# Kernel tuning notes

Measured on AMD Instinct MI355X. Metric: run time of the kernel, lower is better.

Reference implementation:

```python
import jax, jax.numpy as jnp
import numpy as np

N, F_IN, F_OUT, H = 4096, 128, 64, 8
NEG_SLOPE = 0.2

def leaky_relu(x):
    return jnp.where(x >= 0, x, NEG_SLOPE * x)

def setup_inputs() -> dict:
    key = jax.random.key(0)
    k = jax.random.split(key, 6)
    x = jax.random.normal(k[0], (N, F_IN), dtype=jnp.float32)
    conn = jax.random.uniform(k[1], (N, N)) < 0.1
    conn = conn | jnp.eye(N, dtype=bool)
    topology = jnp.where(conn, 0.0, -1e9).astype(jnp.float32)
    proj = jax.random.normal(k[2], (H, F_IN, F_OUT), dtype=jnp.float32) * (1.0 / np.sqrt(F_IN))
    score_src = jax.random.normal(k[3], (H, F_OUT), dtype=jnp.float32) * (1.0 / np.sqrt(F_OUT))
    score_dst = jax.random.normal(k[4], (H, F_OUT), dtype=jnp.float32) * (1.0 / np.sqrt(F_OUT))
    skip_w = jax.random.normal(k[5], (H * F_OUT, F_IN), dtype=jnp.float32) * (1.0 / np.sqrt(F_IN))
    return {"x": x, "topology": topology, "proj": proj,
            "score_src": score_src, "score_dst": score_dst, "skip_w": skip_w}

def reference(x, topology, proj, score_src, score_dst, skip_w):
    # dropout is identity at inference time
    # projected node features: [H, N, F_OUT]
    h = jnp.einsum('ni,hio->hno', x, proj)
    # additive attention scores (GAT): [H, N, 1] + [H, 1, N] -> [H, N, N]
    s_src = jnp.einsum('hno,ho->hn', h, score_src)
    s_dst = jnp.einsum('hno,ho->hn', h, score_dst)
    scores = leaky_relu(s_src[:, :, None] + s_dst[:, None, :])
    attn = jax.nn.softmax(scores + topology[None, :, :], axis=-1)  # [H, N, N]
    # aggregate neighbors, then transpose heads to [N, H, F_OUT]
    out = jnp.einsum('hij,hjo->iho', attn, h)
    # skip connection (F_OUT != F_IN -> projected skip)
    out = out + (x @ skip_w.T).reshape(N, H, F_OUT)
    # mean over heads (concat_heads=False), then LeakyReLU activation
    out = leaky_relu(jnp.mean(out, axis=1))  # [N, F_OUT]
    return out
```

## Files before the change

kernel.cpp:

```cpp
#include <hip/hip_runtime.h>
#include <hip/hip_bf16.h>

#define NN 4096
#define FIN 128
#define FOUT 64
#define NH 8
#define KS 4
#define QT 32

typedef float f32x4 __attribute__((ext_vector_type(4)));
typedef __bf16 bf16x8 __attribute__((ext_vector_type(8)));
typedef unsigned long long u64;

__global__ __launch_bounds__(256) void wc_kernel(
    const float* __restrict__ proj, const float* __restrict__ score_src,
    const float* __restrict__ score_dst, const float* __restrict__ skip_w,
    float* __restrict__ Wc) {
    int idx = blockIdx.x * 256 + threadIdx.x;
    if (idx >= FIN * 80) return;
    int i = idx / 80, c = idx % 80;
    float v = 0.f;
    if (c < 16) {
        int h = c & 7;
        const float* w = (c < 8 ? score_src : score_dst) + h * FOUT;
        const float* p = proj + (size_t)h * FIN * FOUT + (size_t)i * FOUT;
        for (int f = 0; f < FOUT; ++f) v += p[f] * w[f];
    } else {
        int f = c - 16;
        for (int h = 0; h < NH; ++h) v += skip_w[(size_t)(h * FOUT + f) * FIN + i];
        v *= 0.125f;
    }
    Wc[i * 80 + c] = v;
}

__global__ __launch_bounds__(256) void scores_kernel(
    const float* __restrict__ x, const float* __restrict__ Wc,
    float* __restrict__ skipm, unsigned* __restrict__ EF, float2* __restrict__ C12,
    __hip_bfloat16* __restrict__ xb_) {
    __shared__ float wcs[FIN][80];
    __shared__ float xs[16][FIN + 5];
    const int n0 = blockIdx.x * 16;
    const int tid = threadIdx.x;
    for (int i = tid; i < FIN * 80 / 4; i += 256)
        ((float4*)&wcs[0][0])[i] = ((const float4*)Wc)[i];
    const float4* xsrc = (const float4*)(x + (size_t)n0 * FIN);
    for (int i = tid; i < 16 * FIN / 4; i += 256) {
        int r = i >> 5, c4 = i & 31;
        *(float4*)&xs[r][c4 * 4] = xsrc[i];
    }
    __syncthreads();
    const int r = tid & 15;
    const int g = tid >> 4;
    float acc[4];
    float sa = 0.f;
#pragma unroll
    for (int j = 0; j < 4; ++j) acc[j] = 0.f;
#pragma unroll 4
    for (int i = 0; i < FIN; ++i) {
        float xv = xs[r][i];
        float4 p = *(float4*)&wcs[i][16 + g * 4];
        float qv = wcs[i][g];
        acc[0] += xv * p.x; acc[1] += xv * p.y; acc[2] += xv * p.z; acc[3] += xv * p.w;
        sa += xv * qv;
    }
    int n = n0 + r;
#pragma unroll
    for (int j = 0; j < 4; ++j) skipm[(size_t)n * FOUT + g * 4 + j] = acc[j];
    if (g < 8) {
        C12[g * NN + n] = make_float2(expf(sa), expf(0.2f * sa));
    } else {
        __hip_bfloat16 e0 = __float2bfloat16(expf(sa));
        __hip_bfloat16 f0 = __float2bfloat16(expf(0.2f * sa));
        EF[(g - 8) * NN + n] = ((unsigned)*(unsigned short*)&f0 << 16) | (unsigned)*(unsigned short*)&e0;
    }
    {
        int row = tid >> 4, col0 = (tid & 15) * 8;
        const float* src = &xs[row][col0];
        bf16x8 b0;
#pragma unroll
        for (int j = 0; j < 8; ++j) b0[j] = (__bf16)src[j];
        *(bf16x8*)((__bf16*)xb_ + (size_t)(n0 + row) * FIN + col0) = b0;
    }
}

__global__ __launch_bounds__(256) void mask_kernel(
    const float* __restrict__ topo, u64* __restrict__ mb) {
    const int w = blockIdx.x * 4 + (threadIdx.x >> 6);
    const int lane = threadIdx.x & 63;
    size_t base = (size_t)w * 32;
#pragma unroll 4
    for (int it = 0; it < 32; ++it) {
        size_t u = base + it;
        float t = topo[u * 64 + lane];
        u64 b = __ballot(t > -0.5e9f);
        if (lane == 0) mb[u] = b;
    }
}

__global__ __launch_bounds__(256) void vt_kernel(
    const float* __restrict__ proj, const __hip_bfloat16* __restrict__ xb_,
    __hip_bfloat16* __restrict__ Vt_) {
    __shared__ __bf16 pT[FOUT][FIN + 8];
    const int tid = threadIdx.x;
    const int h = blockIdx.x >> 6;
    const int ng = blockIdx.x & 63;
    const __bf16* xb = (const __bf16*)xb_;
    __bf16* Vt = (__bf16*)Vt_;
    for (int idx = tid; idx < FIN * FOUT; idx += 256) {
        int i = idx >> 6, f = idx & 63;
        pT[f][i] = (__bf16)proj[(size_t)h * FIN * FOUT + idx];
    }
    __syncthreads();
    const int wave = tid >> 6, lane = tid & 63, q = lane >> 4, li = lane & 15;
    const int nb = ng * 64 + wave * 16;
    f32x4 acc[4];
#pragma unroll
    for (int n = 0; n < 4; ++n) acc[n] = (f32x4){0.f, 0.f, 0.f, 0.f};
#pragma unroll
    for (int kt = 0; kt < 4; ++kt) {
        bf16x8 bfrag = *(const bf16x8*)(xb + (size_t)(nb + li) * FIN + kt * 32 + q * 8);
#pragma unroll
        for (int ft = 0; ft < 4; ++ft) {
            bf16x8 afrag = *(const bf16x8*)&pT[ft * 16 + li][kt * 32 + q * 8];
            acc[ft] = __builtin_amdgcn_mfma_f32_16x16x32_bf16(afrag, bfrag, acc[ft], 0, 0, 0);
        }
    }
#pragma unroll
    for (int ft = 0; ft < 4; ++ft)
#pragma unroll
        for (int reg = 0; reg < 4; ++reg)
            Vt[((size_t)h * FOUT + ft * 16 + q * 4 + reg) * NN + nb + li] = (__bf16)acc[ft][reg];
}

__attribute__((amdgpu_waves_per_eu(4, 4)))
__global__ __launch_bounds__(512) void attn_kernel(
    const u64* __restrict__ maskbits, const __hip_bfloat16* __restrict__ Vt_,
    const unsigned* __restrict__ EFg, const float2* __restrict__ C12g,
    __hip_bfloat16* __restrict__ accP, float* __restrict__ rsP) {
    __shared__ u64 maskS[QT][17];
    const int tid = threadIdx.x;
    const int h = tid >> 6;
    const int lane = tid & 63, q = lane >> 4, li = lane & 15;
    const int qt = blockIdx.x >> 2, ks = blockIdx.x & 3;
    const int row0 = qt * QT;
    const int kb0 = ks * 1024;

    {
        int r = tid >> 4, wd = tid & 15;
        maskS[r][wd] = maskbits[(size_t)(row0 + r) * 64 + ks * 16 + wd];
    }
    __syncthreads();

    const __bf16* vb = (const __bf16*)Vt_ + (size_t)h * (FOUT * NN) + kb0;
    const unsigned* efb = EFg + (size_t)h * NN + kb0;
    float C1[2], C2[2];
#pragma unroll
    for (int rt = 0; rt < 2; ++rt) {
        float2 c = C12g[(size_t)h * NN + row0 + rt * 16 + li];
        C1[rt] = c.x; C2[rt] = c.y;
    }

    f32x4 acc[2][4];
#pragma unroll
    for (int rt = 0; rt < 2; ++rt)
#pragma unroll
        for (int n = 0; n < 4; ++n) acc[rt][n] = (f32x4){0.f, 0.f, 0.f, 0.f};
    float rs[2] = {0.f, 0.f};

#pragma unroll 1
    for (int kt = 0; kt < 32; ++kt) {
        const unsigned* ep = efb + kt * 32 + q * 8;
        uint4 ea = *(const uint4*)ep;
        uint4 eb = *(const uint4*)(ep + 4);
        bf16x8 vf[4];
#pragma unroll
        for (int n = 0; n < 4; ++n)
            vf[n] = *(const bf16x8*)(vb + (size_t)(n * 16 + li) * NN + kt * 32 + q * 8);
        unsigned ew[8] = {ea.x, ea.y, ea.z, ea.w, eb.x, eb.y, eb.z, eb.w};
#pragma unroll
        for (int rt = 0; rt < 2; ++rt) {
            u64 mw = maskS[rt * 16 + li][kt >> 1];
            unsigned mm = (unsigned)(mw >> ((kt & 1) * 32 + q * 8)) & 0xffu;
            bf16x8 pf;
#pragma unroll
            for (int j = 0; j < 8; ++j) {
                unsigned e = ew[j];
                float E = __uint_as_float(e << 16);
                float F = __uint_as_float(e & 0xffff0000u);
                float pv = fmaxf(C1[rt] * E, C2[rt] * F);
                pv = ((mm >> j) & 1u) ? pv : 0.f;
                rs[rt] += pv;
                pf[j] = (__bf16)pv;
            }
#pragma unroll
            for (int n = 0; n < 4; ++n)
                acc[rt][n] = __builtin_amdgcn_mfma_f32_16x16x32_bf16(pf, vf[n], acc[rt][n], 0, 0, 0);
        }
    }

#pragma unroll
    for (int rt = 0; rt < 2; ++rt) {
        float r = rs[rt];
        r += __shfl_xor(r, 16);
        r += __shfl_xor(r, 32);
        if (q == 0) rsP[(size_t)(ks * NH + h) * NN + row0 + rt * 16 + li] = r;
        __hip_bfloat16* ap = accP + ((size_t)(ks * NH + h) * NN + row0 + rt * 16) * 64;
#pragma unroll
        for (int n = 0; n < 4; ++n)
#pragma unroll
            for (int reg = 0; reg < 4; ++reg)
                ap[(q * 4 + reg) * 64 + n * 16 + li] = __float2bfloat16(acc[rt][n][reg]);
    }
}

__global__ __launch_bounds__(256) void combine_kernel(
    const __hip_bfloat16* __restrict__ accP, const float* __restrict__ rsP,
    float* __restrict__ out) {
    int idx = blockIdx.x * 256 + threadIdx.x;
    int row = idx >> 6, f = idx & 63;
    float s = 0.f;
#pragma unroll 1
    for (int h = 0; h < NH; ++h) {
        float a = 0.f, r = 0.f;
#pragma unroll
        for (int k = 0; k < KS; ++k) {
            a += __bfloat162float(accP[((size_t)(k * NH + h) * NN + row) * 64 + f]);
            r += rsP[(size_t)(k * NH + h) * NN + row];
        }
        s += a / r;
    }
    float v = s * 0.125f + out[idx];
    out[idx] = fmaxf(v, 0.2f * v);
}

extern "C" void kernel_launch(void* const* d_in, const int* in_sizes, int n_in,
                              void* d_out, int out_size, void* d_ws, size_t ws_size,
                              hipStream_t stream) {
    (void)in_sizes; (void)n_in; (void)out_size; (void)ws_size;
    const float* x         = (const float*)d_in[0];
    const float* topology  = (const float*)d_in[1];
    const float* proj      = (const float*)d_in[2];
    const float* score_src = (const float*)d_in[3];
    const float* score_dst = (const float*)d_in[4];
    const float* skip_w    = (const float*)d_in[5];
    float* out = (float*)d_out;

    char* ws = (char*)d_ws;
    __hip_bfloat16* xb = (__hip_bfloat16*)ws;
    __hip_bfloat16* Vt = (__hip_bfloat16*)(ws + 1048576);
    unsigned* EF  = (unsigned*)(ws + 5242880);
    float2* C12   = (float2*)(ws + 5373952);
    float* Wc     = (float*)(ws + 5636096);
    u64* maskbits = (u64*)(ws + 5677056);
    float* rsP    = (float*)(ws + 7774208);
    __hip_bfloat16* accP = (__hip_bfloat16*)(ws + 8298496);
    float* skipm = out;

    wc_kernel<<<40, 256, 0, stream>>>(proj, score_src, score_dst, skip_w, Wc);
    scores_kernel<<<256, 256, 0, stream>>>(x, Wc, skipm, EF, C12, xb);
    mask_kernel<<<2048, 256, 0, stream>>>(topology, maskbits);
    vt_kernel<<<512, 256, 0, stream>>>(proj, xb, Vt);
    attn_kernel<<<512, 512, 0, stream>>>(maskbits, Vt, EF, C12, accP, rsP);
    combine_kernel<<<1024, 256, 0, stream>>>(accP, rsP, out);
}
```

Measured before the change: 209.5 us.

## Fuse mask bit-packing into attention kernel and double-buffer K-tile loads

Removes the separate mask_kernel: each attention block now reads its 32x1024 slice of the fp32 topology directly and ballots it into shared-memory bitmasks, so the packed mask buffer no longer makes a round trip through global memory and one launch is dropped. The main K loop is also software-pipelined with two register buffers, so the EF and V loads for the next tile are issued before the current tile's compute. The risks are higher register pressure under the fixed waves-per-eu setting, and the topology read now sitting serialized at the start of every attention block (64 iterations per wave, unroll 1). Workspace offsets are compacted to match.

```diff
diff --git a/kernel.cpp b/kernel.cpp
--- a/kernel.cpp
+++ b/kernel.cpp
@@ -83,20 +83,6 @@
     }
 }
 
-__global__ __launch_bounds__(256) void mask_kernel(
-    const float* __restrict__ topo, u64* __restrict__ mb) {
-    const int w = blockIdx.x * 4 + (threadIdx.x >> 6);
-    const int lane = threadIdx.x & 63;
-    size_t base = (size_t)w * 32;
-#pragma unroll 4
-    for (int it = 0; it < 32; ++it) {
-        size_t u = base + it;
-        float t = topo[u * 64 + lane];
-        u64 b = __ballot(t > -0.5e9f);
-        if (lane == 0) mb[u] = b;
-    }
-}
-
 __global__ __launch_bounds__(256) void vt_kernel(
     const float* __restrict__ proj, const __hip_bfloat16* __restrict__ xb_,
     __hip_bfloat16* __restrict__ Vt_) {
@@ -134,7 +120,7 @@
 
 __attribute__((amdgpu_waves_per_eu(4, 4)))
 __global__ __launch_bounds__(512) void attn_kernel(
-    const u64* __restrict__ maskbits, const __hip_bfloat16* __restrict__ Vt_,
+    const float* __restrict__ topo, const __hip_bfloat16* __restrict__ Vt_,
     const unsigned* __restrict__ EFg, const float2* __restrict__ C12g,
     __hip_bfloat16* __restrict__ accP, float* __restrict__ rsP) {
     __shared__ u64 maskS[QT][17];
@@ -146,8 +132,14 @@
     const int kb0 = ks * 1024;
 
     {
-        int r = tid >> 4, wd = tid & 15;
-        maskS[r][wd] = maskbits[(size_t)(row0 + r) * 64 + ks * 16 + wd];
+        const float* tpb = topo + (size_t)row0 * NN + kb0;
+#pragma unroll 1
+        for (int it = 0; it < 64; ++it) {
+            int w0 = h * 64 + it;
+            float t = tpb[(size_t)(w0 >> 4) * NN + (w0 & 15) * 64 + lane];
+            u64 b = __ballot(t > -0.5e9f);
+            if (lane == 0) maskS[w0 >> 4][w0 & 15] = b;
+        }
     }
     __syncthreads();
 
@@ -167,16 +159,18 @@
         for (int n = 0; n < 4; ++n) acc[rt][n] = (f32x4){0.f, 0.f, 0.f, 0.f};
     float rs[2] = {0.f, 0.f};
 
-#pragma unroll 1
-    for (int kt = 0; kt < 32; ++kt) {
-        const unsigned* ep = efb + kt * 32 + q * 8;
-        uint4 ea = *(const uint4*)ep;
-        uint4 eb = *(const uint4*)(ep + 4);
-        bf16x8 vf[4];
-#pragma unroll
-        for (int n = 0; n < 4; ++n)
-            vf[n] = *(const bf16x8*)(vb + (size_t)(n * 16 + li) * NN + kt * 32 + q * 8);
-        unsigned ew[8] = {ea.x, ea.y, ea.z, ea.w, eb.x, eb.y, eb.z, eb.w};
+    auto loadc = [&](int kw, uint4& a, uint4& b, bf16x8* v) {
+        const unsigned* ep = efb + kw * 32 + q * 8;
+        a = *(const uint4*)ep;
+        b = *(const uint4*)(ep + 4);
+        const __bf16* vp = vb + (size_t)li * NN + kw * 32 + q * 8;
+        v[0] = *(const bf16x8*)(vp);
+        v[1] = *(const bf16x8*)(vp + 16 * NN);
+        v[2] = *(const bf16x8*)(vp + 32 * NN);
+        v[3] = *(const bf16x8*)(vp + 48 * NN);
+    };
+    auto comp = [&](int kt, const uint4& a, const uint4& b, const bf16x8* v) {
+        unsigned ew[8] = {a.x, a.y, a.z, a.w, b.x, b.y, b.z, b.w};
 #pragma unroll
         for (int rt = 0; rt < 2; ++rt) {
             u64 mw = maskS[rt * 16 + li][kt >> 1];
@@ -194,8 +188,19 @@
             }
 #pragma unroll
             for (int n = 0; n < 4; ++n)
-                acc[rt][n] = __builtin_amdgcn_mfma_f32_16x16x32_bf16(pf, vf[n], acc[rt][n], 0, 0, 0);
-        }
+                acc[rt][n] = __builtin_amdgcn_mfma_f32_16x16x32_bf16(pf, v[n], acc[rt][n], 0, 0, 0);
+        }
+    };
+
+    uint4 a0, b0, a1, b1;
+    bf16x8 v0[4], v1[4];
+    loadc(0, a0, b0, v0);
+#pragma unroll 1
+    for (int kt = 0; kt < 32; kt += 2) {
+        loadc(kt + 1, a1, b1, v1);
+        comp(kt, a0, b0, v0);
+        loadc((kt + 2) & 31, a0, b0, v0);
+        comp(kt + 1, a1, b1, v1);
     }
 
 #pragma unroll
@@ -251,15 +256,13 @@
     unsigned* EF  = (unsigned*)(ws + 5242880);
     float2* C12   = (float2*)(ws + 5373952);
     float* Wc     = (float*)(ws + 5636096);
-    u64* maskbits = (u64*)(ws + 5677056);
-    float* rsP    = (float*)(ws + 7774208);
-    __hip_bfloat16* accP = (__hip_bfloat16*)(ws + 8298496);
+    float* rsP    = (float*)(ws + 5677056);
+    __hip_bfloat16* accP = (__hip_bfloat16*)(ws + 6201344);
     float* skipm = out;
 
     wc_kernel<<<40, 256, 0, stream>>>(proj, score_src, score_dst, skip_w, Wc);
     scores_kernel<<<256, 256, 0, stream>>>(x, Wc, skipm, EF, C12, xb);
-    mask_kernel<<<2048, 256, 0, stream>>>(topology, maskbits);
     vt_kernel<<<512, 256, 0, stream>>>(proj, xb, Vt);
-    attn_kernel<<<512, 512, 0, stream>>>(maskbits, Vt, EF, C12, accP, rsP);
+    attn_kernel<<<512, 512, 0, stream>>>(topology, Vt, EF, C12, accP, rsP);
     combine_kernel<<<1024, 256, 0, stream>>>(accP, rsP, out);
 }
```

After: 228.2 us. 8.9% more time.

## Fuse adjacency mask bit-packing into attention kernel and double key split

Applied to the files above, without the earlier changes.

Removes the separate mask kernel: each attention block now reads its slice of the dense topology and ballots it into shared-memory bitmasks directly. The number of key splits doubles from 4 to 8, so each block covers 512 keys and twice as many blocks launch. The waves-per-EU hint is loosened. This saves a launch and the intermediate bitmask round trip, and the topology streaming can overlap with attention compute. The cost is more partial results for the combine step, and the topology reads now happen inside the latency-sensitive attention kernel.

```diff
diff --git a/kernel.cpp b/kernel.cpp
--- a/kernel.cpp
+++ b/kernel.cpp
@@ -5,7 +5,7 @@
 #define FIN 128
 #define FOUT 64
 #define NH 8
-#define KS 4
+#define KS 8
 #define QT 32
 
 typedef float f32x4 __attribute__((ext_vector_type(4)));
@@ -83,20 +83,6 @@
     }
 }
 
-__global__ __launch_bounds__(256) void mask_kernel(
-    const float* __restrict__ topo, u64* __restrict__ mb) {
-    const int w = blockIdx.x * 4 + (threadIdx.x >> 6);
-    const int lane = threadIdx.x & 63;
-    size_t base = (size_t)w * 32;
-#pragma unroll 4
-    for (int it = 0; it < 32; ++it) {
-        size_t u = base + it;
-        float t = topo[u * 64 + lane];
-        u64 b = __ballot(t > -0.5e9f);
-        if (lane == 0) mb[u] = b;
-    }
-}
-
 __global__ __launch_bounds__(256) void vt_kernel(
     const float* __restrict__ proj, const __hip_bfloat16* __restrict__ xb_,
     __hip_bfloat16* __restrict__ Vt_) {
@@ -132,22 +118,39 @@
             Vt[((size_t)h * FOUT + ft * 16 + q * 4 + reg) * NN + nb + li] = (__bf16)acc[ft][reg];
 }
 
-__attribute__((amdgpu_waves_per_eu(4, 4)))
+__attribute__((amdgpu_waves_per_eu(5)))
 __global__ __launch_bounds__(512) void attn_kernel(
-    const u64* __restrict__ maskbits, const __hip_bfloat16* __restrict__ Vt_,
+    const float* __restrict__ topo, const __hip_bfloat16* __restrict__ Vt_,
     const unsigned* __restrict__ EFg, const float2* __restrict__ C12g,
     __hip_bfloat16* __restrict__ accP, float* __restrict__ rsP) {
-    __shared__ u64 maskS[QT][17];
+    __shared__ u64 maskS[QT][9];
     const int tid = threadIdx.x;
     const int h = tid >> 6;
     const int lane = tid & 63, q = lane >> 4, li = lane & 15;
-    const int qt = blockIdx.x >> 2, ks = blockIdx.x & 3;
+    const int qt = blockIdx.x >> 3, ks = blockIdx.x & 7;
     const int row0 = qt * QT;
-    const int kb0 = ks * 1024;
+    const int kb0 = ks * 512;
 
     {
-        int r = tid >> 4, wd = tid & 15;
-        maskS[r][wd] = maskbits[(size_t)(row0 + r) * 64 + ks * 16 + wd];
+        const float* tpb = topo + (size_t)row0 * NN + kb0;
+#pragma unroll 1
+        for (int it = 0; it < 32; it += 4) {
+            int w0 = h * 32 + it;
+            float t0 = tpb[(size_t)((w0 + 0) >> 3) * NN + ((w0 + 0) & 7) * 64 + lane];
+            float t1 = tpb[(size_t)((w0 + 1) >> 3) * NN + ((w0 + 1) & 7) * 64 + lane];
+            float t2 = tpb[(size_t)((w0 + 2) >> 3) * NN + ((w0 + 2) & 7) * 64 + lane];
+            float t3 = tpb[(size_t)((w0 + 3) >> 3) * NN + ((w0 + 3) & 7) * 64 + lane];
+            u64 b0 = __ballot(t0 > -0.5e9f);
+            u64 b1 = __ballot(t1 > -0.5e9f);
+            u64 b2 = __ballot(t2 > -0.5e9f);
+            u64 b3 = __ballot(t3 > -0.5e9f);
+            if (lane == 0) {
+                maskS[(w0 + 0) >> 3][(w0 + 0) & 7] = b0;
+                maskS[(w0 + 1) >> 3][(w0 + 1) & 7] = b1;
+                maskS[(w0 + 2) >> 3][(w0 + 2) & 7] = b2;
+                maskS[(w0 + 3) >> 3][(w0 + 3) & 7] = b3;
+            }
+        }
     }
     __syncthreads();
 
@@ -168,7 +171,7 @@
     float rs[2] = {0.f, 0.f};
 
 #pragma unroll 1
-    for (int kt = 0; kt < 32; ++kt) {
+    for (int kt = 0; kt < 16; ++kt) {
         const unsigned* ep = efb + kt * 32 + q * 8;
         uint4 ea = *(const uint4*)ep;
         uint4 eb = *(const uint4*)(ep + 4);
@@ -251,15 +254,13 @@
     unsigned* EF  = (unsigned*)(ws + 5242880);
     float2* C12   = (float2*)(ws + 5373952);
     float* Wc     = (float*)(ws + 5636096);
-    u64* maskbits = (u64*)(ws + 5677056);
-    float* rsP    = (float*)(ws + 7774208);
-    __hip_bfloat16* accP = (__hip_bfloat16*)(ws + 8298496);
+    float* rsP    = (float*)(ws + 5677056);
+    __hip_bfloat16* accP = (__hip_bfloat16*)(ws + 6725632);
     float* skipm = out;
 
     wc_kernel<<<40, 256, 0, stream>>>(proj, score_src, score_dst, skip_w, Wc);
     scores_kernel<<<256, 256, 0, stream>>>(x, Wc, skipm, EF, C12, xb);
-    mask_kernel<<<2048, 256, 0, stream>>>(topology, maskbits);
     vt_kernel<<<512, 256, 0, stream>>>(proj, xb, Vt);
-    attn_kernel<<<512, 512, 0, stream>>>(maskbits, Vt, EF, C12, accP, rsP);
+    attn_kernel<<<1024, 512, 0, stream>>>(topology, Vt, EF, C12, accP, rsP);
     combine_kernel<<<1024, 256, 0, stream>>>(accP, rsP, out);
 }
```

Measured after the change: 201.1 us. 1.04x faster.

## Double-buffer V tiles via global_load_lds and split attention across more blocks

Applied to the files above, without the earlier changes.

The attention kernel now stages V tiles into LDS with direct global-to-LDS DMA loads, double-buffered so the next tile's load overlaps the current tile's MFMA work. The key split goes from 4 to 8 and each block handles 4 heads instead of 8, quadrupling the grid size with smaller blocks. This aims to hide global load latency and raise occupancy. In exchange it adds twice as many partial results for combine to reduce, relies on a hand-written vmcnt wait, and issues one redundant DMA of a wrapped tile on the last iteration.

```diff
diff --git a/kernel.cpp b/kernel.cpp
--- a/kernel.cpp
+++ b/kernel.cpp
@@ -5,7 +5,7 @@
 #define FIN 128
 #define FOUT 64
 #define NH 8
-#define KS 4
+#define KS 8
 #define QT 32
 
 typedef float f32x4 __attribute__((ext_vector_type(4)));
@@ -83,20 +83,6 @@
     }
 }
 
-__global__ __launch_bounds__(256) void mask_kernel(
-    const float* __restrict__ topo, u64* __restrict__ mb) {
-    const int w = blockIdx.x * 4 + (threadIdx.x >> 6);
-    const int lane = threadIdx.x & 63;
-    size_t base = (size_t)w * 32;
-#pragma unroll 4
-    for (int it = 0; it < 32; ++it) {
-        size_t u = base + it;
-        float t = topo[u * 64 + lane];
-        u64 b = __ballot(t > -0.5e9f);
-        if (lane == 0) mb[u] = b;
-    }
-}
-
 __global__ __launch_bounds__(256) void vt_kernel(
     const float* __restrict__ proj, const __hip_bfloat16* __restrict__ xb_,
     __hip_bfloat16* __restrict__ Vt_) {
@@ -132,34 +118,65 @@
             Vt[((size_t)h * FOUT + ft * 16 + q * 4 + reg) * NN + nb + li] = (__bf16)acc[ft][reg];
 }
 
-__attribute__((amdgpu_waves_per_eu(4, 4)))
-__global__ __launch_bounds__(512) void attn_kernel(
+__global__ __launch_bounds__(256) void mask_kernel(
+    const float* __restrict__ topo, u64* __restrict__ mb) {
+    const int w = blockIdx.x * 4 + (threadIdx.x >> 6);
+    const int lane = threadIdx.x & 63;
+    size_t base = (size_t)w * 32;
+#pragma unroll 4
+    for (int it = 0; it < 32; ++it) {
+        size_t u = base + it;
+        float t = topo[u * 64 + lane];
+        u64 b = __ballot(t > -0.5e9f);
+        if (lane == 0) mb[u] = b;
+    }
+}
+
+__attribute__((amdgpu_waves_per_eu(4)))
+__global__ __launch_bounds__(256) void attn_kernel(
     const u64* __restrict__ maskbits, const __hip_bfloat16* __restrict__ Vt_,
     const unsigned* __restrict__ EFg, const float2* __restrict__ C12g,
     __hip_bfloat16* __restrict__ accP, float* __restrict__ rsP) {
-    __shared__ u64 maskS[QT][17];
+    __shared__ u64 maskS[QT][9];
+    __shared__ char vA[4][4096];
+    __shared__ char vB[4][4096];
     const int tid = threadIdx.x;
-    const int h = tid >> 6;
+    const int w = tid >> 6;
     const int lane = tid & 63, q = lane >> 4, li = lane & 15;
-    const int qt = blockIdx.x >> 2, ks = blockIdx.x & 3;
+    const int qt = blockIdx.x >> 4, ks = (blockIdx.x >> 1) & 7, hb = blockIdx.x & 1;
+    const int h = hb * 4 + w;
     const int row0 = qt * QT;
-    const int kb0 = ks * 1024;
-
-    {
-        int r = tid >> 4, wd = tid & 15;
-        maskS[r][wd] = maskbits[(size_t)(row0 + r) * 64 + ks * 16 + wd];
-    }
-    __syncthreads();
+    const int kb0 = ks * 512;
+
+    const int r_ = lane >> 2;
+    const int sg = ((lane & 3) - (r_ >> 1)) & 3;
+    const size_t laneoff = (size_t)r_ * NN + sg * 8;
+    const int rdoff = li * 64 + ((q + (li >> 1)) & 3) * 16;
 
     const __bf16* vb = (const __bf16*)Vt_ + (size_t)h * (FOUT * NN) + kb0;
     const unsigned* efb = EFg + (size_t)h * NN + kb0;
+
+#define DMA_TILE(DST, KT) do {                                                     \
+    _Pragma("unroll")                                                              \
+    for (int c = 0; c < 4; ++c) {                                                  \
+        const __bf16* g_ = vb + (size_t)c * (16 * NN) + (KT) * 32 + laneoff;       \
+        __builtin_amdgcn_global_load_lds(                                          \
+            (const __attribute__((address_space(1))) void*)g_,                     \
+            (__attribute__((address_space(3))) void*)&DST[w][c * 1024], 16, 0, 0); \
+    }                                                                              \
+} while (0)
+
+    DMA_TILE(vA, 0);
+    { int rr = tid >> 3, wd = tid & 7;
+      maskS[rr][wd] = maskbits[(size_t)(row0 + rr) * 64 + ks * 8 + wd]; }
+    __syncthreads();
+
     float C1[2], C2[2];
 #pragma unroll
     for (int rt = 0; rt < 2; ++rt) {
         float2 c = C12g[(size_t)h * NN + row0 + rt * 16 + li];
         C1[rt] = c.x; C2[rt] = c.y;
     }
-
     f32x4 acc[2][4];
 #pragma unroll
     for (int rt = 0; rt < 2; ++rt)
@@ -167,36 +184,47 @@
         for (int n = 0; n < 4; ++n) acc[rt][n] = (f32x4){0.f, 0.f, 0.f, 0.f};
     float rs[2] = {0.f, 0.f};
 
+#define CHUNK_BODY(SRC, DSTN, KT) do {                                                        \
+    const unsigned* ep_ = efb + (KT) * 32 + q * 8;                                            \
+    uint4 ea_ = *(const uint4*)ep_;                                                           \
+    uint4 eb_ = *(const uint4*)(ep_ + 4);                                                     \
+    asm volatile("" ::: "memory");                           \
+    DMA_TILE(DSTN, ((KT) + 1) & 15);                                                          \
+    asm volatile("s_waitcnt vmcnt(4)" ::: "memory");                                          \
+    bf16x8 vf_[4];                                                                            \
+    _Pragma("unroll")                                                                         \
+    for (int n = 0; n < 4; ++n)                                                               \
+        vf_[n] = *(const bf16x8*)&SRC[w][n * 1024 + rdoff];                                   \
+    unsigned ew_[8] = {ea_.x, ea_.y, ea_.z, ea_.w, eb_.x, eb_.y, eb_.z, eb_.w};               \
+    _Pragma("unroll")                                                                         \
+    for (int rt = 0; rt < 2; ++rt) {                                                          \
+        u64 mw_ = maskS[rt * 16 + li][(KT) >> 1];                                             \
+        unsigned mm_ = (unsigned)(mw_ >> (((KT) & 1) * 32 + q * 8)) & 0xffu;                  \
+        bf16x8 pf_;                                                                           \
+        _Pragma("unroll")                                                                     \
+        for (int j = 0; j < 8; ++j) {                                                         \
+            unsigned e_ = ew_[j];                                                             \
+            float E_ = __uint_as_float(e_ << 16);                                             \
+            float F_ = __uint_as_float(e_ & 0xffff0000u);                                     \
+            float pv_ = fmaxf(C1[rt] * E_, C2[rt] * F_);                                      \
+            pv_ = ((mm_ >> j) & 1u) ? pv_ : 0.f;                                              \
+            rs[rt] += pv_;                                                                    \
+            pf_[j] = (__bf16)pv_;                                                             \
+        }                                                                                     \
+        _Pragma("unroll")                                                                     \
+        for (int n = 0; n < 4; ++n)                                                           \
+            acc[rt][n] = __builtin_amdgcn_mfma_f32_16x16x32_bf16(pf_, vf_[n], acc[rt][n],     \
+                                                                 0, 0, 0);                    \
+    }                                                                                         \
+} while (0)
+
 #pragma unroll 1
-    for (int kt = 0; kt < 32; ++kt) {
-        const unsigned* ep = efb + kt * 32 + q * 8;
-        uint4 ea = *(const uint4*)ep;
-        uint4 eb = *(const uint4*)(ep + 4);
-        bf16x8 vf[4];
-#pragma unroll
-        for (int n = 0; n < 4; ++n)
-            vf[n] = *(const bf16x8*)(vb + (size_t)(n * 16 + li) * NN + kt * 32 + q * 8);
-        unsigned ew[8] = {ea.x, ea.y, ea.z, ea.w, eb.x, eb.y, eb.z, eb.w};
-#pragma unroll
-        for (int rt = 0; rt < 2; ++rt) {
-            u64 mw = maskS[rt * 16 + li][kt >> 1];
-            unsigned mm = (unsigned)(mw >> ((kt & 1) * 32 + q * 8)) & 0xffu;
-            bf16x8 pf;
-#pragma unroll
-            for (int j = 0; j < 8; ++j) {
-                unsigned e = ew[j];
-                float E = __uint_as_float(e << 16);
-                float F = __uint_as_float(e & 0xffff0000u);
-                float pv = fmaxf(C1[rt] * E, C2[rt] * F);
-                pv = ((mm >> j) & 1u) ? pv : 0.f;
-                rs[rt] += pv;
-                pf[j] = (__bf16)pv;
-            }
-#pragma unroll
-            for (int n = 0; n < 4; ++n)
-                acc[rt][n] = __builtin_amdgcn_mfma_f32_16x16x32_bf16(pf, vf[n], acc[rt][n], 0, 0, 0);
-        }
-    }
+    for (int kt = 0; kt < 16; kt += 2) {
+        CHUNK_BODY(vA, vB, kt);
+        CHUNK_BODY(vB, vA, kt + 1);
+    }
+#undef CHUNK_BODY
+#undef DMA_TILE
 
 #pragma unroll
     for (int rt = 0; rt < 2; ++rt) {
@@ -253,13 +281,13 @@
     float* Wc     = (float*)(ws + 5636096);
     u64* maskbits = (u64*)(ws + 5677056);
     float* rsP    = (float*)(ws + 7774208);
-    __hip_bfloat16* accP = (__hip_bfloat16*)(ws + 8298496);
+    __hip_bfloat16* accP = (__hip_bfloat16*)(ws + 8822784);
     float* skipm = out;
 
     wc_kernel<<<40, 256, 0, stream>>>(proj, score_src, score_dst, skip_w, Wc);
     scores_kernel<<<256, 256, 0, stream>>>(x, Wc, skipm, EF, C12, xb);
+    vt_kernel<<<512, 256, 0, stream>>>(proj, xb, Vt);
     mask_kernel<<<2048, 256, 0, stream>>>(topology, maskbits);
-    vt_kernel<<<512, 256, 0, stream>>>(proj, xb, Vt);
-    attn_kernel<<<512, 512, 0, stream>>>(maskbits, Vt, EF, C12, accP, rsP);
+    attn_kernel<<<2048, 256, 0, stream>>>(maskbits, Vt, EF, C12, accP, rsP);
     combine_kernel<<<1024, 256, 0, stream>>>(accP, rsP, out);
 }
```

New measurement: 187.5 us. -10.5%, faster.
